# Kernel tuning notes

Hardware: AMD Instinct MI355X
Metric: run time of the kernel (lower is better)

## Reference

```python
import jax, jax.numpy as jnp
import numpy as np

N, E = 20000, 320000          # nodes, edges (avg in-degree ~16)
F_IN, EMB, T, OUT = 40, 40, 5, 2
F_T = EMB // T                # per-tower output width = 8
EPS_STD, EPS_GN = 1e-5, 1e-5


def _lin_init(k, fan_in, fan_out, extra=()):
    return jax.random.normal(k, (*extra, fan_in, fan_out), jnp.float32) / np.sqrt(fan_in)


def setup_inputs() -> dict:
    key = jax.random.key(0)
    ks = jax.random.split(key, 8)
    # deg histogram in init: all 20000 nodes with degree 16 -> avg_deg['log'] = log(16+1)
    return dict(
        x=jax.random.normal(ks[0], (N, F_IN), jnp.float32),
        edge_index=jax.random.randint(ks[1], (2, E), 0, N),
        W_pre=_lin_init(ks[2], 2 * F_IN, F_IN, (T,)),   # per-tower pre-MLP
        b_pre=jnp.zeros((T, F_IN), jnp.float32),
        W_post=_lin_init(ks[3], 13 * F_IN, F_T, (T,)),  # (4 agg * 3 scalers + 1 residual) * F_in
        b_post=jnp.zeros((T, F_T), jnp.float32),
        W_lin=_lin_init(ks[4], T * F_T, EMB),           # PNAConv final mixing linear
        b_lin=jnp.zeros((EMB,), jnp.float32),
        gn_weight=jnp.ones((EMB,), jnp.float32),
        gn_bias=jnp.zeros((EMB,), jnp.float32),
        gn_mean_scale=jnp.ones((EMB,), jnp.float32),
        W1=_lin_init(ks[5], EMB, EMB),                  # head hidden linear
        b1=jnp.zeros((EMB,), jnp.float32),
        W2=_lin_init(ks[6], EMB, OUT),                  # head output linear
        b2=jnp.zeros((OUT,), jnp.float32),
        avg_deg_log=jnp.float32(np.log(17.0)),
    )


def _pna_conv(x, src, dst, W_pre, b_pre, W_post, b_post, W_lin, b_lin, avg_deg_log):
    xi, xj = x[dst], x[src]                              # gather: [E, F]
    h = jnp.concatenate([xi, xj], axis=-1)               # [E, 2F]
    m = jnp.einsum('ef,tfg->etg', h, W_pre) + b_pre      # per-tower messages [E, T, F]
    cnt = jax.ops.segment_sum(jnp.ones((E,), m.dtype), dst, num_segments=N)  # in-degree [N]
    denom = jnp.maximum(cnt, 1.0)[:, None, None]
    mean = jax.ops.segment_sum(m, dst, num_segments=N) / denom
    mean2 = jax.ops.segment_sum(m * m, dst, num_segments=N) / denom
    std = jnp.sqrt(jax.nn.relu(mean2 - mean * mean) + EPS_STD)
    has = (cnt > 0)[:, None, None]
    mn = jnp.where(has, jax.ops.segment_min(m, dst, num_segments=N), 0.0)
    mx = jnp.where(has, jax.ops.segment_max(m, dst, num_segments=N), 0.0)
    agg = jnp.concatenate([mean, mn, mx, std], axis=-1)  # [N, T, 4F]
    deg = jnp.maximum(cnt, 1.0)[:, None, None]
    logd = jnp.log(deg + 1.0)
    out = jnp.concatenate(
        [agg, agg * (logd / avg_deg_log), agg * (avg_deg_log / logd)], axis=-1)  # [N, T, 12F]
    out = jnp.concatenate(
        [jnp.broadcast_to(x[:, None, :], (N, T, x.shape[-1])), out], axis=-1)    # [N, T, 13F]
    out = jnp.einsum('ntf,tfg->ntg', out, W_post) + b_post                       # [N, T, F_T]
    return out.reshape(N, T * F_T) @ W_lin + b_lin


def _graph_norm(x, w, b, mean_scale):
    mean = jnp.mean(x, axis=0, keepdims=True)
    out = x - mean_scale * mean
    var = jnp.mean(out * out, axis=0, keepdims=True)
    return w * out / jnp.sqrt(var + EPS_GN) + b


def reference(x, edge_index, W_pre, b_pre, W_post, b_post, W_lin, b_lin,
              gn_weight, gn_bias, gn_mean_scale, W1, b1, W2, b2, avg_deg_log):
    src, dst = edge_index[0], edge_index[1]
    h = _pna_conv(x, src, dst, W_pre, b_pre, W_post, b_post, W_lin, b_lin, avg_deg_log)
    h = jax.nn.relu(_graph_norm(h, gn_weight, gn_bias, gn_mean_scale))
    h = jax.nn.relu(h @ W1 + b1)   # dropout_rate=None -> no dropout
    return h @ W2 + b2
```

## Files before the change

### kernel.cpp

```cpp
#include <hip/hip_runtime.h>
#include <math.h>

#define N_NODES 20000
#define N_EDGES 320000
#define F_IN 40
#define T_TOW 5
#define EMB 40
#define NPB_PRE 16
#define NBLK_MIX 313
#define NBLK_POST 79
#define PLANE (T_TOW * N_NODES * 40)
#define ECHUNK 16
#define STRIDE 64

typedef __attribute__((ext_vector_type(8))) _Float16 half8;
typedef __attribute__((ext_vector_type(2))) _Float16 half2_t;

#define WS_STATS   0
#define WS_CURSOR  320
#define WS_SSRC    80384
#define WS_MS      5200384
#define WS_MD      13200384
#define WS_AGG     21200384
#define WS_XPOST   53200384
#define WS_POSTT   56400384
#define WS_H0T     69200384
#define WS_PART    72400384

__global__ __launch_bounds__(256) void k_pre(const float* __restrict__ x,
                                             const float* __restrict__ W_pre,
                                             const float* __restrict__ b_pre,
                                             const float* __restrict__ W_post,
                                             const float* __restrict__ b_post,
                                             _Float16* __restrict__ mS,
                                             _Float16* __restrict__ mD,
                                             float* __restrict__ xpostT,
                                             int* __restrict__ cursor) {
  const int tid = threadIdx.x;
  const int n0 = blockIdx.x * NPB_PRE;
  if (tid < NPB_PRE) cursor[n0 + tid] = (n0 + tid) * STRIDE;
  const bool statlane = tid < 200;
  const int q = tid - 200;
  const bool xplane = (q >= 0 && q < 40);
  const int tc = statlane ? tid : 199;
  const int t = tc / 40, g = tc - t * 40;
  const int t2 = xplane ? q / 8 : 0, g2 = xplane ? q - (q / 8) * 8 : 0;
  float wA[40], wB[40];
  const float* Wt = W_pre + t * 3200;
#pragma unroll
  for (int j = 0; j < 40; ++j) {
    wA[j] = statlane ? Wt[j * 40 + g] : W_post[t2 * 4160 + j * 8 + g2];
    wB[j] = statlane ? Wt[(40 + j) * 40 + g] : 0.f;
  }
  const float bias = statlane ? b_pre[t * 40 + g] : b_post[t2 * 8 + g2];
  for (int ni = 0; ni < NPB_PRE; ++ni) {
    const int n = n0 + ni;
    const float* xr = x + n * F_IN;
    float aA = bias, aB = 0.f;
#pragma unroll
    for (int j = 0; j < 40; j += 4) {
      const float4 xv = *(const float4*)(xr + j);
      aA += xv.x * wA[j] + xv.y * wA[j + 1] + xv.z * wA[j + 2] + xv.w * wA[j + 3];
      aB += xv.x * wB[j] + xv.y * wB[j + 1] + xv.z * wB[j + 2] + xv.w * wB[j + 3];
    }
    if (statlane) {
      mD[n * 200 + tc] = (_Float16)aA;
      mS[n * 200 + tc] = (_Float16)aB;
    } else if (xplane) {
      xpostT[t2 * (N_NODES * 8) + n * 8 + g2] = aA;
    }
  }
}

__global__ __launch_bounds__(256) void k_scatter(const int* __restrict__ src,
                                                 const int* __restrict__ dst,
                                                 int* __restrict__ cursor,
                                                 int* __restrict__ ssrc) {
  int i = blockIdx.x * 256 + threadIdx.x;
  if (i < N_EDGES) {
    int d = dst[i];
    int pos = atomicAdd(&cursor[d], 1);
    ssrc[pos] = src[i];
  }
}

__global__ __launch_bounds__(256) void k_edge(const _Float16* __restrict__ mS,
                                              const _Float16* __restrict__ mD,
                                              const int* __restrict__ cursor,
                                              const int* __restrict__ ssrc,
                                              _Float16* __restrict__ aggS) {
  const int lane = threadIdx.x & 63;
  const int wv = threadIdx.x >> 6;
  const int n = blockIdx.x * 4 + wv;
  const int r0 = n * STRIDE;
  const int r1 = __builtin_amdgcn_readfirstlane(cursor[n]);
  const int cnt = r1 - r0;
  const int cpa = lane;
  const bool bact = lane < 36;
  const int cpb = bact ? 64 + lane : 99;
  const half2_t mda = ((const half2_t*)(mD + n * 200))[cpa];
  const half2_t mdb = ((const half2_t*)(mD + n * 200))[cpb];

  const _Float16 HINF = (_Float16)65504.f;
  half2_t suma = {0, 0}, ssqa = {0, 0}, sumb = {0, 0}, ssqb = {0, 0};
  half2_t mna = {HINF, HINF}, mxa = {-HINF, -HINF};
  half2_t mnb = {HINF, HINF}, mxb = {-HINF, -HINF};
  half2_t va = {0, 0}, vb = {0, 0};

  if (cnt > 0) {
    for (int p = r0; p < r1; p += ECHUNK) {
      half2_t ha[ECHUNK], hb[ECHUNK];
#pragma unroll
      for (int i = 0; i < ECHUNK; ++i) {
        const int qe = (p + i < r1) ? (p + i) : (r1 - 1);
        const int s = __builtin_amdgcn_readfirstlane(ssrc[qe]);
        const half2_t* row = (const half2_t*)(mS + s * 200);
        ha[i] = row[cpa];
        hb[i] = row[cpb];
      }
#pragma unroll
      for (int i = 0; i < ECHUNK; ++i) {
        suma += ha[i];
        ssqa += ha[i] * ha[i];
        mna = __builtin_elementwise_min(mna, ha[i]);
        mxa = __builtin_elementwise_max(mxa, ha[i]);
        sumb += hb[i];
        ssqb += hb[i] * hb[i];
        mnb = __builtin_elementwise_min(mnb, hb[i]);
        mxb = __builtin_elementwise_max(mxb, hb[i]);
      }
      va = ha[ECHUNK - 1];
      vb = hb[ECHUNK - 1];
    }
  }

  const int padded = ((cnt + ECHUNK - 1) / ECHUNK) * ECHUNK;
  const float d = (float)(padded - cnt);
  const float inv = (cnt > 0) ? 1.f / (float)cnt : 0.f;
#pragma unroll
  for (int set = 0; set < 2; ++set) {
    if (set == 1 && !bact) break;
    const int cp = set == 0 ? cpa : cpb;
    const half2_t sum2 = set == 0 ? suma : sumb;
    const half2_t ssq2 = set == 0 ? ssqa : ssqb;
    const half2_t mn2 = set == 0 ? mna : mnb;
    const half2_t mx2 = set == 0 ? mxa : mxb;
    const half2_t vl2 = set == 0 ? va : vb;
    const half2_t md2 = set == 0 ? mda : mdb;
    half2_t omean, omn, omx, osd;
#pragma unroll
    for (int j = 0; j < 2; ++j) {
      float mean, mnf, mxf, sd;
      if (cnt > 0) {
        const float vl = (float)vl2[j];
        const float sf = (float)sum2[j] - d * vl;
        const float qf = (float)ssq2[j] - d * vl * vl;
        const float msm = sf * inv;
        const float var = qf * inv - msm * msm;
        sd = sqrtf(fmaxf(var, 0.f) + 1e-5f);
        const float mdf = (float)md2[j];
        mean = mdf + msm;
        mnf = mdf + (float)mn2[j];
        mxf = mdf + (float)mx2[j];
      } else {
        mean = 0.f; mnf = 0.f; mxf = 0.f; sd = sqrtf(1e-5f);
      }
      omean[j] = (_Float16)mean;
      omn[j] = (_Float16)mnf;
      omx[j] = (_Float16)mxf;
      osd[j] = (_Float16)sd;
    }
    const int t = cp / 20, g = 2 * (cp - t * 20);
    half2_t* a = (half2_t*)(aggS + (t * N_NODES + n) * 40 + g);
    a[0] = omean;
    *(half2_t*)((_Float16*)a + PLANE) = omn;
    *(half2_t*)((_Float16*)a + 2 * PLANE) = omx;
    *(half2_t*)((_Float16*)a + 3 * PLANE) = osd;
  }
}

__global__ __launch_bounds__(256) void k_post(const _Float16* __restrict__ aggS,
                                              const int* __restrict__ cursor,
                                              const float* __restrict__ W_post,
                                              const float* __restrict__ avg_dl,
                                              float* __restrict__ postT4) {
  __shared__ _Float16 sAgg[256 * 42];
  const int t = blockIdx.y;
  const int s = blockIdx.z;
  const int tid = threadIdx.x;
  const int n0 = blockIdx.x * 256;
  const _Float16* gsrc = aggS + s * PLANE + (t * N_NODES + n0) * 40;
  const int lim = (N_NODES - n0) * 40;
  for (int i = 0; i < 40; ++i) {
    const int idx = tid + i * 256;
    const _Float16 vv = (idx < lim) ? gsrc[idx] : (_Float16)0.f;
    sAgg[(idx / 40) * 42 + (idx - (idx / 40) * 40)] = vv;
  }
  __syncthreads();
  const int n = n0 + tid;
  const bool ok = n < N_NODES;
  const int nn = ok ? n : N_NODES - 1;
  const int cnt = cursor[nn] - nn * STRIDE;
  const float degf = fmaxf((float)cnt, 1.f);
  const float logd = logf(degf + 1.f);
  const float avg = avg_dl[0];
  const float s1 = logd / avg, s2 = avg / logd;
  const float* Wt = W_post + t * 4160;
  float acc[8];
#pragma unroll
  for (int g2 = 0; g2 < 8; ++g2) acc[g2] = 0.f;
  const _Float16* myrow = sAgg + tid * 42;
  for (int i = 0; i < 5; ++i) {
#pragma unroll
    for (int jj = 0; jj < 8; ++jj) {
      const int kj = s * 40 + i * 8 + jj;
      const float val = (float)myrow[i * 8 + jj];
      const float* wa = Wt + (40 + kj) * 8;
      const float* wb = Wt + (200 + kj) * 8;
      const float* wc = Wt + (360 + kj) * 8;
#pragma unroll
      for (int g2 = 0; g2 < 8; ++g2)
        acc[g2] += val * (wa[g2] + s1 * wb[g2] + s2 * wc[g2]);
    }
  }
  if (ok) {
    float* pr = postT4 + ((s * T_TOW + t) * N_NODES + n) * 8;
    float4 o0 = {acc[0], acc[1], acc[2], acc[3]};
    float4 o1 = {acc[4], acc[5], acc[6], acc[7]};
    *(float4*)(pr) = o0;
    *(float4*)(pr + 4) = o1;
  }
}

__global__ __launch_bounds__(256) void k_mix(const float* __restrict__ postT4,
                                             const float* __restrict__ xpostT,
                                             const float* __restrict__ W_lin,
                                             const float* __restrict__ b_lin,
                                             float* __restrict__ h0T,
                                             float* __restrict__ partial) {
  __shared__ float sP[64 * 41];
  const int tid = threadIdx.x;
  const int n0 = blockIdx.x * 64;
  for (int i = 0; i < 10; ++i) {
    const int idx = tid + i * 256;
    const int tt = idx >> 9;
    const int r = idx & 511;
    const int row = r >> 3, c = r & 7;
    const int nn0 = n0 + row;
    const int nn = (nn0 < N_NODES) ? nn0 : 0;
    float val = xpostT[tt * (N_NODES * 8) + nn * 8 + c];
#pragma unroll
    for (int s = 0; s < 4; ++s)
      val += postT4[((s * T_TOW + tt) * N_NODES + nn) * 8 + c];
    sP[row * 41 + tt * 8 + c] = (nn0 < N_NODES) ? val : 0.f;
  }
  __syncthreads();
  const int wv = tid >> 6, lane = tid & 63;
  const int n = n0 + lane;
  const bool ok = n < N_NODES;
  for (int c = wv; c < 5; c += 4) {
    const int c0 = c * 8;
    const float4 bb0 = *(const float4*)(b_lin + c0);
    const float4 bb1 = *(const float4*)(b_lin + c0 + 4);
    float a0 = bb0.x, a1 = bb0.y, a2 = bb0.z, a3 = bb0.w;
    float a4 = bb1.x, a5 = bb1.y, a6 = bb1.z, a7 = bb1.w;
    for (int k = 0; k < 40; ++k) {
      const float p = sP[lane * 41 + k];
      const float* w = W_lin + k * EMB + c0;
      const float4 w0 = *(const float4*)(w);
      const float4 w1 = *(const float4*)(w + 4);
      a0 = fmaf(p, w0.x, a0); a1 = fmaf(p, w0.y, a1);
      a2 = fmaf(p, w0.z, a2); a3 = fmaf(p, w0.w, a3);
      a4 = fmaf(p, w1.x, a4); a5 = fmaf(p, w1.y, a5);
      a6 = fmaf(p, w1.z, a6); a7 = fmaf(p, w1.w, a7);
    }
    if (ok) {
      h0T[(c0 + 0) * N_NODES + n] = a0;
      h0T[(c0 + 1) * N_NODES + n] = a1;
      h0T[(c0 + 2) * N_NODES + n] = a2;
      h0T[(c0 + 3) * N_NODES + n] = a3;
      h0T[(c0 + 4) * N_NODES + n] = a4;
      h0T[(c0 + 5) * N_NODES + n] = a5;
      h0T[(c0 + 6) * N_NODES + n] = a6;
      h0T[(c0 + 7) * N_NODES + n] = a7;
    } else {
      a0 = a1 = a2 = a3 = a4 = a5 = a6 = a7 = 0.f;
    }
    float s[8] = {a0, a1, a2, a3, a4, a5, a6, a7};
#pragma unroll
    for (int j = 0; j < 8; ++j) {
      float sv = s[j], qv = s[j] * s[j];
#pragma unroll
      for (int m = 32; m >= 1; m >>= 1) {
        sv += __shfl_xor(sv, m, 64);
        qv += __shfl_xor(qv, m, 64);
      }
      if (lane == 0) {
        partial[blockIdx.x * 80 + c0 + j] = sv;
        partial[blockIdx.x * 80 + 40 + c0 + j] = qv;
      }
    }
  }
}

__global__ __launch_bounds__(64) void k_stats(const float* __restrict__ partial,
                                              float* __restrict__ S1,
                                              float* __restrict__ S2) {
  const int col = blockIdx.x;
  const int lane = threadIdx.x;
  float s = 0.f;
  for (int b = lane; b < NBLK_MIX; b += 64) s += partial[b * 80 + col];
#pragma unroll
  for (int m = 32; m >= 1; m >>= 1) s += __shfl_xor(s, m, 64);
  if (lane == 0) {
    if (col < 40) S1[col] = s;
    else S2[col - 40] = s;
  }
}

__global__ __launch_bounds__(256) void k_head(const float* __restrict__ h0T,
                                              const float* __restrict__ S1,
                                              const float* __restrict__ S2,
                                              const float* __restrict__ gn_w,
                                              const float* __restrict__ gn_b,
                                              const float* __restrict__ gn_ms,
                                              const float* __restrict__ W1,
                                              const float* __restrict__ b1,
                                              const float* __restrict__ W2,
                                              const float* __restrict__ b2,
                                              float* __restrict__ out) {
  __shared__ float sV[64 * 41];
  __shared__ float sH[64 * 41];
  const int tid = threadIdx.x;
  const int n0 = blockIdx.x * 64;
  const float invN = 1.f / (float)N_NODES;
  for (int i = 0; i < 10; ++i) {
    const int idx = tid + i * 256;
    const int e = idx >> 6, r = idx & 63;
    const int nn0 = n0 + r;
    const int nn = (nn0 < N_NODES) ? nn0 : 0;
    const float M = S1[e] * invN;
    const float ms = gn_ms[e];
    const float var = S2[e] * invN - ms * (2.f - ms) * M * M;
    const float sc = gn_w[e] / sqrtf(var + 1e-5f);
    const float he = h0T[e * N_NODES + nn];
    sV[r * 41 + e] = fmaxf((he - ms * M) * sc + gn_b[e], 0.f);
  }
  __syncthreads();
  const int wv = tid >> 6, lane = tid & 63;
  const int c0 = wv * 10;
  float acc[10];
#pragma unroll
  for (int j = 0; j < 10; ++j) acc[j] = b1[c0 + j];
  for (int k = 0; k < 40; ++k) {
    const float p = sV[lane * 41 + k];
    const float* w = W1 + k * EMB + c0;
#pragma unroll
    for (int j = 0; j < 10; ++j) acc[j] = fmaf(p, w[j], acc[j]);
  }
#pragma unroll
  for (int j = 0; j < 10; ++j) sH[lane * 41 + c0 + j] = fmaxf(acc[j], 0.f);
  __syncthreads();
  if (tid < 64) {
    const int n = n0 + tid;
    if (n < N_NODES) {
      float o0 = b2[0], o1 = b2[1];
      const float* hr = sH + tid * 41;
#pragma unroll
      for (int k = 0; k < 40; ++k) {
        const float r = hr[k];
        o0 = fmaf(r, W2[k * 2], o0);
        o1 = fmaf(r, W2[k * 2 + 1], o1);
      }
      out[n * 2] = o0;
      out[n * 2 + 1] = o1;
    }
  }
}

extern "C" void kernel_launch(void* const* d_in, const int* in_sizes, int n_in,
                              void* d_out, int out_size, void* d_ws, size_t ws_size,
                              hipStream_t stream) {
  const float* x      = (const float*)d_in[0];
  const int*   ei     = (const int*)d_in[1];
  const float* W_pre  = (const float*)d_in[2];
  const float* b_pre  = (const float*)d_in[3];
  const float* W_post = (const float*)d_in[4];
  const float* b_post = (const float*)d_in[5];
  const float* W_lin  = (const float*)d_in[6];
  const float* b_lin  = (const float*)d_in[7];
  const float* gn_w   = (const float*)d_in[8];
  const float* gn_b   = (const float*)d_in[9];
  const float* gn_ms  = (const float*)d_in[10];
  const float* W1     = (const float*)d_in[11];
  const float* b1     = (const float*)d_in[12];
  const float* W2     = (const float*)d_in[13];
  const float* b2     = (const float*)d_in[14];
  const float* avg_dl = (const float*)d_in[15];
  float* out = (float*)d_out;

  char* ws = (char*)d_ws;
  float* S1   = (float*)(ws + WS_STATS);
  float* S2   = S1 + 40;
  int* cursor = (int*)(ws + WS_CURSOR);
  int* ssrc   = (int*)(ws + WS_SSRC);
  _Float16* mS   = (_Float16*)(ws + WS_MS);
  _Float16* mD   = (_Float16*)(ws + WS_MD);
  _Float16* aggS = (_Float16*)(ws + WS_AGG);
  float* xpostT  = (float*)(ws + WS_XPOST);
  float* postT4  = (float*)(ws + WS_POSTT);
  float* h0T     = (float*)(ws + WS_H0T);
  float* part    = (float*)(ws + WS_PART);
  const int* e_src = ei;
  const int* e_dst = ei + N_EDGES;

  k_pre<<<N_NODES / NPB_PRE, 256, 0, stream>>>(x, W_pre, b_pre, W_post, b_post,
                                               mS, mD, xpostT, cursor);
  k_scatter<<<(N_EDGES + 255) / 256, 256, 0, stream>>>(e_src, e_dst, cursor, ssrc);
  k_edge<<<N_NODES / 4, 256, 0, stream>>>(mS, mD, cursor, ssrc, aggS);
  k_post<<<dim3(NBLK_POST, T_TOW, 4), 256, 0, stream>>>(aggS, cursor, W_post,
                                                        avg_dl, postT4);
  k_mix<<<NBLK_MIX, 256, 0, stream>>>(postT4, xpostT, W_lin, b_lin, h0T, part);
  k_stats<<<80, 64, 0, stream>>>(part, S1, S2);
  k_head<<<NBLK_MIX, 256, 0, stream>>>(h0T, S1, S2, gn_w, gn_b, gn_ms,
                                       W1, b1, W2, b2, out);
}
```

Baseline: 221.3 us.

## Fuse post-aggregation projection into mixing kernel and fold stats into head

Merges k_post and k_mix into one k_postmix kernel. Each wave handles one aggregator plane for 64 nodes, loads its fp16 aggregate rows directly as half8 vectors with next-tower prefetch, and leaves per-tower projections in shared memory instead of writing postT4 to global. k_stats is removed: every head block now re-reduces the 313×80 partial sums itself. This cuts two launches and the postT4 round trip, but each head block repeats the small global reduction and the per-thread register load in postmix grows.

```diff
diff --git a/kernel.cpp b/kernel.cpp
--- a/kernel.cpp
+++ b/kernel.cpp
@@ -8,7 +8,6 @@
 #define EMB 40
 #define NPB_PRE 16
 #define NBLK_MIX 313
-#define NBLK_POST 79
 #define PLANE (T_TOW * N_NODES * 40)
 #define ECHUNK 16
 #define STRIDE 64
@@ -23,7 +22,6 @@
 #define WS_MD      13200384
 #define WS_AGG     21200384
 #define WS_XPOST   53200384
-#define WS_POSTT   56400384
 #define WS_H0T     69200384
 #define WS_PART    72400384
 
@@ -179,85 +177,81 @@
   }
 }
 
-__global__ __launch_bounds__(256) void k_post(const _Float16* __restrict__ aggS,
-                                              const int* __restrict__ cursor,
-                                              const float* __restrict__ W_post,
-                                              const float* __restrict__ avg_dl,
-                                              float* __restrict__ postT4) {
-  __shared__ _Float16 sAgg[256 * 42];
-  const int t = blockIdx.y;
-  const int s = blockIdx.z;
+__global__ __launch_bounds__(256) void k_postmix(const _Float16* __restrict__ aggS,
+                                                 const int* __restrict__ cursor,
+                                                 const float* __restrict__ W_post,
+                                                 const float* __restrict__ avg_dl,
+                                                 const float* __restrict__ xpostT,
+                                                 const float* __restrict__ W_lin,
+                                                 const float* __restrict__ b_lin,
+                                                 float* __restrict__ h0T,
+                                                 float* __restrict__ partial) {
+  __shared__ float sPost[4][64 * 41];
+  __shared__ float sP[64 * 41];
   const int tid = threadIdx.x;
-  const int n0 = blockIdx.x * 256;
-  const _Float16* gsrc = aggS + s * PLANE + (t * N_NODES + n0) * 40;
-  const int lim = (N_NODES - n0) * 40;
-  for (int i = 0; i < 40; ++i) {
-    const int idx = tid + i * 256;
-    const _Float16 vv = (idx < lim) ? gsrc[idx] : (_Float16)0.f;
-    sAgg[(idx / 40) * 42 + (idx - (idx / 40) * 40)] = vv;
-  }
-  __syncthreads();
-  const int n = n0 + tid;
+  const int wv = tid >> 6, lane = tid & 63;
+  const int n0 = blockIdx.x * 64;
+  const int n = n0 + lane;
   const bool ok = n < N_NODES;
   const int nn = ok ? n : N_NODES - 1;
+  const int st = __builtin_amdgcn_readfirstlane(wv);
   const int cnt = cursor[nn] - nn * STRIDE;
   const float degf = fmaxf((float)cnt, 1.f);
   const float logd = logf(degf + 1.f);
   const float avg = avg_dl[0];
-  const float s1 = logd / avg, s2 = avg / logd;
-  const float* Wt = W_post + t * 4160;
-  float acc[8];
-#pragma unroll
-  for (int g2 = 0; g2 < 8; ++g2) acc[g2] = 0.f;
-  const _Float16* myrow = sAgg + tid * 42;
-  for (int i = 0; i < 5; ++i) {
-#pragma unroll
-    for (int jj = 0; jj < 8; ++jj) {
-      const int kj = s * 40 + i * 8 + jj;
-      const float val = (float)myrow[i * 8 + jj];
-      const float* wa = Wt + (40 + kj) * 8;
-      const float* wb = Wt + (200 + kj) * 8;
-      const float* wc = Wt + (360 + kj) * 8;
-#pragma unroll
-      for (int g2 = 0; g2 < 8; ++g2)
-        acc[g2] += val * (wa[g2] + s1 * wb[g2] + s2 * wc[g2]);
-    }
-  }
-  if (ok) {
-    float* pr = postT4 + ((s * T_TOW + t) * N_NODES + n) * 8;
-    float4 o0 = {acc[0], acc[1], acc[2], acc[3]};
-    float4 o1 = {acc[4], acc[5], acc[6], acc[7]};
-    *(float4*)(pr) = o0;
-    *(float4*)(pr + 4) = o1;
-  }
-}
-
-__global__ __launch_bounds__(256) void k_mix(const float* __restrict__ postT4,
-                                             const float* __restrict__ xpostT,
-                                             const float* __restrict__ W_lin,
-                                             const float* __restrict__ b_lin,
-                                             float* __restrict__ h0T,
-                                             float* __restrict__ partial) {
-  __shared__ float sP[64 * 41];
-  const int tid = threadIdx.x;
-  const int n0 = blockIdx.x * 64;
+  const float s1v = logd / avg, s2v = avg / logd;
+
+  half8 cur[5], nx[5];
+  {
+    const half8* ar = (const half8*)(aggS + st * PLANE + nn * 40);
+#pragma unroll
+    for (int q2 = 0; q2 < 5; ++q2) cur[q2] = ar[q2];
+  }
+  for (int t = 0; t < 5; ++t) {
+    if (t < 4) {
+      const half8* ar = (const half8*)(aggS + st * PLANE + ((t + 1) * N_NODES + nn) * 40);
+#pragma unroll
+      for (int q2 = 0; q2 < 5; ++q2) nx[q2] = ar[q2];
+    }
+    const float* Wt = W_post + t * 4160 + (40 + st * 40) * 8;
+    float A[8], B[8], C[8];
+#pragma unroll
+    for (int g = 0; g < 8; ++g) { A[g] = 0.f; B[g] = 0.f; C[g] = 0.f; }
+#pragma unroll
+    for (int f = 0; f < 40; ++f) {
+      const float val = (float)cur[f >> 3][f & 7];
+      const float* wrow = Wt + f * 8;
+#pragma unroll
+      for (int g = 0; g < 8; ++g) {
+        A[g] = fmaf(val, wrow[g], A[g]);
+        B[g] = fmaf(val, wrow[1280 + g], B[g]);
+        C[g] = fmaf(val, wrow[2560 + g], C[g]);
+      }
+    }
+    float* dstp = &sPost[st][lane * 41 + t * 8];
+#pragma unroll
+    for (int g = 0; g < 8; ++g) dstp[g] = A[g] + s1v * B[g] + s2v * C[g];
+    if (t < 4) {
+#pragma unroll
+      for (int q2 = 0; q2 < 5; ++q2) cur[q2] = nx[q2];
+    }
+  }
+  __syncthreads();
+
+#pragma unroll
   for (int i = 0; i < 10; ++i) {
-    const int idx = tid + i * 256;
-    const int tt = idx >> 9;
-    const int r = idx & 511;
-    const int row = r >> 3, c = r & 7;
-    const int nn0 = n0 + row;
-    const int nn = (nn0 < N_NODES) ? nn0 : 0;
-    float val = xpostT[tt * (N_NODES * 8) + nn * 8 + c];
-#pragma unroll
-    for (int s = 0; s < 4; ++s)
-      val += postT4[((s * T_TOW + tt) * N_NODES + nn) * 8 + c];
-    sP[row * 41 + tt * 8 + c] = (nn0 < N_NODES) ? val : 0.f;
+    const int c = wv + 4 * i;
+    const int t2 = c >> 3, g2 = c & 7;
+    float v = 0.f;
+    if (ok) {
+      v = xpostT[t2 * (N_NODES * 8) + n * 8 + g2]
+        + sPost[0][lane * 41 + c] + sPost[1][lane * 41 + c]
+        + sPost[2][lane * 41 + c] + sPost[3][lane * 41 + c];
+    }
+    sP[lane * 41 + c] = v;
   }
   __syncthreads();
-  const int wv = tid >> 6, lane = tid & 63;
-  const int n = n0 + lane;
-  const bool ok = n < N_NODES;
+
   for (int c = wv; c < 5; c += 4) {
     const int c0 = c * 8;
     const float4 bb0 = *(const float4*)(b_lin + c0);
@@ -286,10 +280,10 @@
     } else {
       a0 = a1 = a2 = a3 = a4 = a5 = a6 = a7 = 0.f;
     }
-    float s[8] = {a0, a1, a2, a3, a4, a5, a6, a7};
+    float red[8] = {a0, a1, a2, a3, a4, a5, a6, a7};
 #pragma unroll
     for (int j = 0; j < 8; ++j) {
-      float sv = s[j], qv = s[j] * s[j];
+      float sv = red[j], qv = red[j] * red[j];
 #pragma unroll
       for (int m = 32; m >= 1; m >>= 1) {
         sv += __shfl_xor(sv, m, 64);
@@ -303,24 +297,8 @@
   }
 }
 
-__global__ __launch_bounds__(64) void k_stats(const float* __restrict__ partial,
-                                              float* __restrict__ S1,
-                                              float* __restrict__ S2) {
-  const int col = blockIdx.x;
-  const int lane = threadIdx.x;
-  float s = 0.f;
-  for (int b = lane; b < NBLK_MIX; b += 64) s += partial[b * 80 + col];
-#pragma unroll
-  for (int m = 32; m >= 1; m >>= 1) s += __shfl_xor(s, m, 64);
-  if (lane == 0) {
-    if (col < 40) S1[col] = s;
-    else S2[col - 40] = s;
-  }
-}
-
-__global__ __launch_bounds__(256) void k_head(const float* __restrict__ h0T,
-                                              const float* __restrict__ S1,
-                                              const float* __restrict__ S2,
+__global__ __launch_bounds__(256) void k_head(const float* __restrict__ partial,
+                                              const float* __restrict__ h0T,
                                               const float* __restrict__ gn_w,
                                               const float* __restrict__ gn_b,
                                               const float* __restrict__ gn_ms,
@@ -331,17 +309,37 @@
                                               float* __restrict__ out) {
   __shared__ float sV[64 * 41];
   __shared__ float sH[64 * 41];
+  __shared__ float sS[3][80];
   const int tid = threadIdx.x;
   const int n0 = blockIdx.x * 64;
   const float invN = 1.f / (float)N_NODES;
+  if (tid < 240) {
+    const int chunk = tid / 80;
+    const int col = tid - chunk * 80;
+    const int b0 = chunk * 105;
+    const int b1 = (chunk == 2) ? NBLK_MIX : b0 + 105;
+    float a0 = 0.f, a1 = 0.f, a2 = 0.f, a3 = 0.f;
+    int b = b0;
+    for (; b + 4 <= b1; b += 4) {
+      a0 += partial[(b + 0) * 80 + col];
+      a1 += partial[(b + 1) * 80 + col];
+      a2 += partial[(b + 2) * 80 + col];
+      a3 += partial[(b + 3) * 80 + col];
+    }
+    for (; b < b1; ++b) a0 += partial[b * 80 + col];
+    sS[chunk][col] = (a0 + a1) + (a2 + a3);
+  }
+  __syncthreads();
   for (int i = 0; i < 10; ++i) {
     const int idx = tid + i * 256;
     const int e = idx >> 6, r = idx & 63;
     const int nn0 = n0 + r;
     const int nn = (nn0 < N_NODES) ? nn0 : 0;
-    const float M = S1[e] * invN;
+    const float S1e = sS[0][e] + sS[1][e] + sS[2][e];
+    const float S2e = sS[0][40 + e] + sS[1][40 + e] + sS[2][40 + e];
+    const float M = S1e * invN;
     const float ms = gn_ms[e];
-    const float var = S2[e] * invN - ms * (2.f - ms) * M * M;
+    const float var = S2e * invN - ms * (2.f - ms) * M * M;
     const float sc = gn_w[e] / sqrtf(var + 1e-5f);
     const float he = h0T[e * N_NODES + nn];
     sV[r * 41 + e] = fmaxf((he - ms * M) * sc + gn_b[e], 0.f);
@@ -400,15 +398,12 @@
   float* out = (float*)d_out;
 
   char* ws = (char*)d_ws;
-  float* S1   = (float*)(ws + WS_STATS);
-  float* S2   = S1 + 40;
   int* cursor = (int*)(ws + WS_CURSOR);
   int* ssrc   = (int*)(ws + WS_SSRC);
   _Float16* mS   = (_Float16*)(ws + WS_MS);
   _Float16* mD   = (_Float16*)(ws + WS_MD);
   _Float16* aggS = (_Float16*)(ws + WS_AGG);
   float* xpostT  = (float*)(ws + WS_XPOST);
-  float* postT4  = (float*)(ws + WS_POSTT);
   float* h0T     = (float*)(ws + WS_H0T);
   float* part    = (float*)(ws + WS_PART);
   const int* e_src = ei;
@@ -418,10 +413,8 @@
                                                mS, mD, xpostT, cursor);
   k_scatter<<<(N_EDGES + 255) / 256, 256, 0, stream>>>(e_src, e_dst, cursor, ssrc);
   k_edge<<<N_NODES / 4, 256, 0, stream>>>(mS, mD, cursor, ssrc, aggS);
-  k_post<<<dim3(NBLK_POST, T_TOW, 4), 256, 0, stream>>>(aggS, cursor, W_post,
-                                                        avg_dl, postT4);
-  k_mix<<<NBLK_MIX, 256, 0, stream>>>(postT4, xpostT, W_lin, b_lin, h0T, part);
-  k_stats<<<80, 64, 0, stream>>>(part, S1, S2);
-  k_head<<<NBLK_MIX, 256, 0, stream>>>(h0T, S1, S2, gn_w, gn_b, gn_ms,
+  k_postmix<<<NBLK_MIX, 256, 0, stream>>>(aggS, cursor, W_post, avg_dl,
+                                          xpostT, W_lin, b_lin, h0T, part);
+  k_head<<<NBLK_MIX, 256, 0, stream>>>(part, h0T, gn_w, gn_b, gn_ms,
                                        W1, b1, W2, b2, out);
 }
```

Measured after the change: 218.4 us. Within noise of the previous version (-1.3%).
